# Performance work log

Hardware: AMD Instinct MI355X
Metric: run time of the kernel (lower is better)

Reference implementation:

```python
import jax, jax.numpy as jnp
import numpy as np

B, L, H = 64, 512, 768   # batch, BERT seq len, BERT hidden
D, S, Q = 16, 64, 32     # max_doc_len (sentences), max_seq_len (tokens/sentence), max_query_len
NEG = -900000.0


def setup_inputs() -> dict:
    key = jax.random.key(0)
    k1, k2, k3, k4, k5 = jax.random.split(key, 5)
    rng = np.random.default_rng(0)
    query_len = rng.integers(8, Q + 1, size=B)                 # actual query lengths
    doc_len = rng.integers(4, D + 1, size=B)                   # sentences per doc
    seq_lens = rng.integers(4, 29, size=(B, D))                # tokens per sentence
    seq_lens[np.arange(D)[None, :] >= doc_len[:, None]] = 0    # zero beyond doc_len
    # layout guarantee: 32 + 2 + 16*28 = 482 <= 512
    return {
        "hidden_states": jax.random.normal(k1, (B, L, H), jnp.float32),
        "W_doc": jax.random.normal(k2, (H, 1), jnp.float32) * 0.02,
        "b_doc": jax.random.normal(k3, (1,), jnp.float32) * 0.02,
        "W_query": jax.random.normal(k4, (H, 1), jnp.float32) * 0.02,
        "b_query": jax.random.normal(k5, (1,), jnp.float32) * 0.02,
        "query_len": jnp.asarray(query_len, jnp.int32),
        "seq_lens": jnp.asarray(seq_lens, jnp.int32),
    }


def reference(hidden_states, W_doc, b_doc, W_query, b_query, query_len, seq_lens):
    # --- ragged sentence extraction (vectorized get_sentence_state) ---
    # sentence j of example i starts at query_len[i] + 2 + sum(seq_lens[i,:j])
    offsets = query_len[:, None] + 2 + jnp.cumsum(seq_lens, axis=1) - seq_lens  # [B,D]
    pos = jnp.arange(S, dtype=jnp.int32)
    idx = jnp.clip(offsets[:, :, None] + pos, 0, L - 1)                         # [B,D,S]
    mask_doc = pos[None, None, :] < seq_lens[:, :, None]                        # [B,D,S] bool
    sent = jnp.take_along_axis(hidden_states, idx.reshape(B, D * S, 1), axis=1)
    sent = sent.reshape(B, D, S, H)
    sent = jnp.where(mask_doc[..., None], sent, 0.0)  # zero padding, as original

    # --- masked softmax attention pooling over tokens in each sentence ---
    alpha = (sent @ W_doc + b_doc)[..., 0]                                      # [B,D,S]
    alpha = jnp.where(mask_doc, alpha, NEG)
    alpha = jax.nn.softmax(alpha, axis=-1)
    doc_pooled = jnp.einsum('bds,bdsh->bdh', alpha, sent)                       # [B,D,H]

    # --- ragged query extraction + pooling ---
    q_state = hidden_states[:, 1:1 + Q]                                         # [B,Q,H]
    mask_q = jnp.arange(Q, dtype=jnp.int32)[None, :] < query_len[:, None]       # [B,Q]
    q_state = jnp.where(mask_q[..., None], q_state, 0.0)
    aq = (q_state @ W_query + b_query)[..., 0]                                  # [B,Q]
    aq = jnp.where(mask_q, aq, NEG)
    aq = jax.nn.softmax(aq, axis=-1)
    q_pooled = jnp.einsum('bq,bqh->bh', aq, q_state)                            # [B,H]
    q_bcast = jnp.broadcast_to(q_pooled[:, None, :], doc_pooled.shape)          # [B,D,H]
    return doc_pooled, q_bcast
```

## Files before the change

kernel.cpp:

```cpp
#include <hip/hip_runtime.h>

namespace {
constexpr int Bn = 64;
constexpr int Ln = 512;
constexpr int Hn = 768;
constexpr int Dn = 16;
constexpr int Qn = 32;
constexpr float NEGV = -900000.0f;
}

template<int NIT>
__device__ __forceinline__ void pool_span(
    const float* __restrict__ rowbase,
    const float* __restrict__ W, float bias, int len,
    float* __restrict__ score_sh, float (*pool_sh)[Hn],
    int t, int wave, int lane, float out3[3])
{
    float4 wv[3];
#pragma unroll
    for (int j = 0; j < 3; ++j)
        wv[j] = *reinterpret_cast<const float4*>(W + (lane + 64 * j) * 4);

    float4 c[NIT][3];
#pragma unroll
    for (int it = 0; it < NIT; ++it) {
        const int s = wave + 4 * it;
        if (s < len) {
            const float* r = rowbase + s * Hn;
#pragma unroll
            for (int j = 0; j < 3; ++j)
                c[it][j] = *reinterpret_cast<const float4*>(r + (lane + 64 * j) * 4);
            float p = c[it][0].x * wv[0].x + c[it][0].y * wv[0].y
                    + c[it][0].z * wv[0].z + c[it][0].w * wv[0].w
                    + c[it][1].x * wv[1].x + c[it][1].y * wv[1].y
                    + c[it][1].z * wv[1].z + c[it][1].w * wv[1].w
                    + c[it][2].x * wv[2].x + c[it][2].y * wv[2].y
                    + c[it][2].z * wv[2].z + c[it][2].w * wv[2].w;
#pragma unroll
            for (int off = 32; off; off >>= 1) p += __shfl_down(p, off);
            if (lane == 0) score_sh[s] = p;
        }
    }
    __syncthreads();

    if (t < Qn) {
        const float raw = (t < len) ? (score_sh[t] + bias) : NEGV;
        float m = raw;
#pragma unroll
        for (int off = 16; off; off >>= 1) m = fmaxf(m, __shfl_xor(m, off, 32));
        const float e = expf(raw - m);
        float den = e;
#pragma unroll
        for (int off = 16; off; off >>= 1) den += __shfl_xor(den, off, 32);
        score_sh[t] = (t < len) ? (e / den) : 0.f;
    }
    __syncthreads();

    float4 acc[3];
#pragma unroll
    for (int j = 0; j < 3; ++j) acc[j] = make_float4(0.f, 0.f, 0.f, 0.f);
#pragma unroll
    for (int it = 0; it < NIT; ++it) {
        const int s = wave + 4 * it;
        if (s < len) {
            const float a = score_sh[s];
#pragma unroll
            for (int j = 0; j < 3; ++j) {
                acc[j].x += a * c[it][j].x;
                acc[j].y += a * c[it][j].y;
                acc[j].z += a * c[it][j].z;
                acc[j].w += a * c[it][j].w;
            }
        }
    }

#pragma unroll
    for (int j = 0; j < 3; ++j)
        *reinterpret_cast<float4*>(&pool_sh[wave][(lane + 64 * j) * 4]) = acc[j];
    __syncthreads();
    out3[0] = pool_sh[0][t]       + pool_sh[1][t]       + pool_sh[2][t]       + pool_sh[3][t];
    out3[1] = pool_sh[0][t + 256] + pool_sh[1][t + 256] + pool_sh[2][t + 256] + pool_sh[3][t + 256];
    out3[2] = pool_sh[0][t + 512] + pool_sh[1][t + 512] + pool_sh[2][t + 512] + pool_sh[3][t + 512];
}

__global__ __launch_bounds__(256) void k_fused(
    const float* __restrict__ hs,
    const float* __restrict__ Wd, const float* __restrict__ bd,
    const float* __restrict__ Wq, const float* __restrict__ bq,
    const int* __restrict__ qlen, const int* __restrict__ slens,
    float* __restrict__ out_doc, float* __restrict__ out_q)
{
    __shared__ float score_sh[Qn];
    __shared__ float pool_sh[4][Hn];

    const int t = threadIdx.x;
    const int wave = t >> 6;
    const int lane = t & 63;
    const int bid = blockIdx.x;

    if (bid < Bn) {
        const int b = bid;
        const int ql = qlen[b];
        const float* bp = hs + ((size_t)b * Ln + 1) * Hn;
        float o3[3];
        pool_span<8>(bp, Wq, bq[0], ql, score_sh, pool_sh, t, wave, lane, o3);
        for (int dd = 0; dd < Dn; ++dd) {
            float* o = out_q + ((size_t)b * Dn + dd) * Hn;
            o[t] = o3[0]; o[t + 256] = o3[1]; o[t + 512] = o3[2];
        }
    } else {
        const int id = bid - Bn;
        const int b = id >> 4;
        const int d = id & 15;

        const int sv = slens[b * Dn + (lane & 15)];
        const int sl = __shfl(sv, d, 64);
        float* o = out_doc + ((size_t)b * Dn + d) * Hn;
        if (sl == 0) {
            o[t] = 0.f; o[t + 256] = 0.f; o[t + 512] = 0.f;
            return;
        }
        int pref = 0;
#pragma unroll
        for (int k = 0; k < Dn; ++k)
            pref += (k < d) ? __shfl(sv, k, 64) : 0;
        const int base = qlen[b] + 2 + pref;
        const float* bp = hs + ((size_t)b * Ln + base) * Hn;
        float o3[3];
        pool_span<7>(bp, Wd, bd[0], sl, score_sh, pool_sh, t, wave, lane, o3);
        o[t] = o3[0]; o[t + 256] = o3[1]; o[t + 512] = o3[2];
    }
}

extern "C" void kernel_launch(void* const* d_in, const int* in_sizes, int n_in,
                              void* d_out, int out_size, void* d_ws, size_t ws_size,
                              hipStream_t stream)
{
    const float* hs    = (const float*)d_in[0];
    const float* Wd    = (const float*)d_in[1];
    const float* bd    = (const float*)d_in[2];
    const float* Wq    = (const float*)d_in[3];
    const float* bq    = (const float*)d_in[4];
    const int*   qlen  = (const int*)d_in[5];
    const int*   slens = (const int*)d_in[6];

    float* out_doc = (float*)d_out;
    float* out_q   = out_doc + (size_t)Bn * Dn * Hn;

    k_fused<<<Bn + Bn * Dn, 256, 0, stream>>>(hs, Wd, bd, Wq, bq,
                                              qlen, slens, out_doc, out_q);
}
```

Before: 16.36 us.

## Replace two-pass softmax pooling with per-wave online softmax and merge

Each wave now keeps a running max, running denominator and rescaled accumulator (flash-style online softmax) while streaming its rows. The per-wave partial results are merged through shared memory with exp weights at the end. This removes the score buffer, one block barrier and the register array that held every loaded row, which should lower register pressure and allow more waves in flight. Output stores become float4, but all four waves now write the same full row, so global write traffic is four times larger and that may offset the gain.

```diff
diff --git a/kernel.cpp b/kernel.cpp
--- a/kernel.cpp
+++ b/kernel.cpp
@@ -5,82 +5,76 @@
 constexpr int Ln = 512;
 constexpr int Hn = 768;
 constexpr int Dn = 16;
-constexpr int Qn = 32;
 constexpr float NEGV = -900000.0f;
 }
 
 template<int NIT>
-__device__ __forceinline__ void pool_span(
+__device__ __forceinline__ void flash_span(
     const float* __restrict__ rowbase,
     const float* __restrict__ W, float bias, int len,
-    float* __restrict__ score_sh, float (*pool_sh)[Hn],
-    int t, int wave, int lane, float out3[3])
+    float4 (*pool4)[192], float* m_sh, float* l_sh,
+    int t, int wave, int lane, float4 out4[3])
 {
     float4 wv[3];
 #pragma unroll
     for (int j = 0; j < 3; ++j)
         wv[j] = *reinterpret_cast<const float4*>(W + (lane + 64 * j) * 4);
 
-    float4 c[NIT][3];
+    float4 acc[3];
+#pragma unroll
+    for (int j = 0; j < 3; ++j) acc[j] = make_float4(0.f, 0.f, 0.f, 0.f);
+    float m = -INFINITY, l = 0.f;
+
 #pragma unroll
     for (int it = 0; it < NIT; ++it) {
         const int s = wave + 4 * it;
         if (s < len) {
             const float* r = rowbase + s * Hn;
+            float4 c0 = *reinterpret_cast<const float4*>(r + lane * 4);
+            float4 c1 = *reinterpret_cast<const float4*>(r + (lane + 64) * 4);
+            float4 c2 = *reinterpret_cast<const float4*>(r + (lane + 128) * 4);
+            float p = c0.x * wv[0].x + c0.y * wv[0].y + c0.z * wv[0].z + c0.w * wv[0].w
+                    + c1.x * wv[1].x + c1.y * wv[1].y + c1.z * wv[1].z + c1.w * wv[1].w
+                    + c2.x * wv[2].x + c2.y * wv[2].y + c2.z * wv[2].z + c2.w * wv[2].w;
 #pragma unroll
-            for (int j = 0; j < 3; ++j)
-                c[it][j] = *reinterpret_cast<const float4*>(r + (lane + 64 * j) * 4);
-            float p = c[it][0].x * wv[0].x + c[it][0].y * wv[0].y
-                    + c[it][0].z * wv[0].z + c[it][0].w * wv[0].w
-                    + c[it][1].x * wv[1].x + c[it][1].y * wv[1].y
-                    + c[it][1].z * wv[1].z + c[it][1].w * wv[1].w
-                    + c[it][2].x * wv[2].x + c[it][2].y * wv[2].y
-                    + c[it][2].z * wv[2].z + c[it][2].w * wv[2].w;
-#pragma unroll
-            for (int off = 32; off; off >>= 1) p += __shfl_down(p, off);
-            if (lane == 0) score_sh[s] = p;
-        }
-    }
-    __syncthreads();
-
-    if (t < Qn) {
-        const float raw = (t < len) ? (score_sh[t] + bias) : NEGV;
-        float m = raw;
-#pragma unroll
-        for (int off = 16; off; off >>= 1) m = fmaxf(m, __shfl_xor(m, off, 32));
-        const float e = expf(raw - m);
-        float den = e;
-#pragma unroll
-        for (int off = 16; off; off >>= 1) den += __shfl_xor(den, off, 32);
-        score_sh[t] = (t < len) ? (e / den) : 0.f;
-    }
-    __syncthreads();
-
-    float4 acc[3];
-#pragma unroll
-    for (int j = 0; j < 3; ++j) acc[j] = make_float4(0.f, 0.f, 0.f, 0.f);
-#pragma unroll
-    for (int it = 0; it < NIT; ++it) {
-        const int s = wave + 4 * it;
-        if (s < len) {
-            const float a = score_sh[s];
-#pragma unroll
-            for (int j = 0; j < 3; ++j) {
-                acc[j].x += a * c[it][j].x;
-                acc[j].y += a * c[it][j].y;
-                acc[j].z += a * c[it][j].z;
-                acc[j].w += a * c[it][j].w;
+            for (int off = 32; off; off >>= 1) p += __shfl_xor(p, off);
+            p += bias;
+            if (p > m) {
+                const float sc = __expf(m - p);
+                acc[0].x *= sc; acc[0].y *= sc; acc[0].z *= sc; acc[0].w *= sc;
+                acc[1].x *= sc; acc[1].y *= sc; acc[1].z *= sc; acc[1].w *= sc;
+                acc[2].x *= sc; acc[2].y *= sc; acc[2].z *= sc; acc[2].w *= sc;
+                l *= sc; m = p;
             }
+            const float e = __expf(p - m);
+            acc[0].x += e * c0.x; acc[0].y += e * c0.y; acc[0].z += e * c0.z; acc[0].w += e * c0.w;
+            acc[1].x += e * c1.x; acc[1].y += e * c1.y; acc[1].z += e * c1.z; acc[1].w += e * c1.w;
+            acc[2].x += e * c2.x; acc[2].y += e * c2.y; acc[2].z += e * c2.z; acc[2].w += e * c2.w;
+            l += e;
         }
     }
 
 #pragma unroll
-    for (int j = 0; j < 3; ++j)
-        *reinterpret_cast<float4*>(&pool_sh[wave][(lane + 64 * j) * 4]) = acc[j];
+    for (int j = 0; j < 3; ++j) pool4[wave][lane + 64 * j] = acc[j];
+    if (lane == 0) { m_sh[wave] = m; l_sh[wave] = l; }
     __syncthreads();
-    out3[0] = pool_sh[0][t]       + pool_sh[1][t]       + pool_sh[2][t]       + pool_sh[3][t];
-    out3[1] = pool_sh[0][t + 256] + pool_sh[1][t + 256] + pool_sh[2][t + 256] + pool_sh[3][t + 256];
-    out3[2] = pool_sh[0][t + 512] + pool_sh[1][t + 512] + pool_sh[2][t + 512] + pool_sh[3][t + 512];
+
+    const float m0 = m_sh[0], m1 = m_sh[1], m2 = m_sh[2], m3 = m_sh[3];
+    const float M = fmaxf(fmaxf(m0, m1), fmaxf(m2, m3));
+    const float w0 = __expf(m0 - M), w1 = __expf(m1 - M),
+                w2 = __expf(m2 - M), w3 = __expf(m3 - M);
+    const float L = l_sh[0] * w0 + l_sh[1] * w1 + l_sh[2] * w2 + l_sh[3] * w3;
+    const float inv = 1.f / L;
+#pragma unroll
+    for (int j = 0; j < 3; ++j) {
+        const int col = lane + 64 * j;
+        const float4 s0 = pool4[0][col], s1 = pool4[1][col],
+                     s2 = pool4[2][col], s3 = pool4[3][col];
+        out4[j].x = (s0.x * w0 + s1.x * w1 + s2.x * w2 + s3.x * w3) * inv;
+        out4[j].y = (s0.y * w0 + s1.y * w1 + s2.y * w2 + s3.y * w3) * inv;
+        out4[j].z = (s0.z * w0 + s1.z * w1 + s2.z * w2 + s3.z * w3) * inv;
+        out4[j].w = (s0.w * w0 + s1.w * w1 + s2.w * w2 + s3.w * w3) * inv;
+    }
 }
 
 __global__ __launch_bounds__(256) void k_fused(
@@ -90,8 +84,8 @@
     const int* __restrict__ qlen, const int* __restrict__ slens,
     float* __restrict__ out_doc, float* __restrict__ out_q)
 {
-    __shared__ float score_sh[Qn];
-    __shared__ float pool_sh[4][Hn];
+    __shared__ float4 pool4[4][192];
+    __shared__ float m_sh[4], l_sh[4];
 
     const int t = threadIdx.x;
     const int wave = t >> 6;
@@ -102,11 +96,13 @@
         const int b = bid;
         const int ql = qlen[b];
         const float* bp = hs + ((size_t)b * Ln + 1) * Hn;
-        float o3[3];
-        pool_span<8>(bp, Wq, bq[0], ql, score_sh, pool_sh, t, wave, lane, o3);
+        float4 o4[3];
+        flash_span<8>(bp, Wq, bq[0], ql, pool4, m_sh, l_sh, t, wave, lane, o4);
         for (int dd = 0; dd < Dn; ++dd) {
-            float* o = out_q + ((size_t)b * Dn + dd) * Hn;
-            o[t] = o3[0]; o[t + 256] = o3[1]; o[t + 512] = o3[2];
+            float4* o = reinterpret_cast<float4*>(out_q + ((size_t)b * Dn + dd) * Hn);
+            o[lane]       = o4[0];
+            o[lane + 64]  = o4[1];
+            o[lane + 128] = o4[2];
         }
     } else {
         const int id = bid - Bn;
@@ -115,9 +111,10 @@
 
         const int sv = slens[b * Dn + (lane & 15)];
         const int sl = __shfl(sv, d, 64);
-        float* o = out_doc + ((size_t)b * Dn + d) * Hn;
+        float4* o = reinterpret_cast<float4*>(out_doc + ((size_t)b * Dn + d) * Hn);
         if (sl == 0) {
-            o[t] = 0.f; o[t + 256] = 0.f; o[t + 512] = 0.f;
+            const float4 z = make_float4(0.f, 0.f, 0.f, 0.f);
+            o[lane] = z; o[lane + 64] = z; o[lane + 128] = z;
             return;
         }
         int pref = 0;
@@ -126,9 +123,11 @@
             pref += (k < d) ? __shfl(sv, k, 64) : 0;
         const int base = qlen[b] + 2 + pref;
         const float* bp = hs + ((size_t)b * Ln + base) * Hn;
-        float o3[3];
-        pool_span<7>(bp, Wd, bd[0], sl, score_sh, pool_sh, t, wave, lane, o3);
-        o[t] = o3[0]; o[t + 256] = o3[1]; o[t + 512] = o3[2];
+        float4 o4[3];
+        flash_span<7>(bp, Wd, bd[0], sl, pool4, m_sh, l_sh, t, wave, lane, o4);
+        o[lane]       = o4[0];
+        o[lane + 64]  = o4[1];
+        o[lane + 128] = o4[2];
     }
 }
 
```

New measurement: 25.05 us. 53.1% more time.

## Use 512-thread blocks, register-shuffle softmax weights, and float4 reductions

Applied to the files above, without the earlier changes.

Doubles the block to 8 waves so each wave loads at most 4 rows instead of 7-8, which lowers per-thread register use and gives more memory requests in flight. Every wave now computes the softmax redundantly and broadcasts alpha with a shuffle, removing one barrier and the shared-memory round trip for the weights. The final cross-wave reduction and the output stores use float4 on 192 threads. The risk is fewer resident blocks per CU and an 8-way shared-memory reduction.

```diff
diff --git a/kernel.cpp b/kernel.cpp
--- a/kernel.cpp
+++ b/kernel.cpp
@@ -5,26 +5,67 @@
 constexpr int Ln = 512;
 constexpr int Hn = 768;
 constexpr int Dn = 16;
-constexpr int Qn = 32;
 constexpr float NEGV = -900000.0f;
 }
 
-template<int NIT>
-__device__ __forceinline__ void pool_span(
-    const float* __restrict__ rowbase,
-    const float* __restrict__ W, float bias, int len,
-    float* __restrict__ score_sh, float (*pool_sh)[Hn],
-    int t, int wave, int lane, float out3[3])
+__global__ __launch_bounds__(512) void k_fused(
+    const float* __restrict__ hs,
+    const float* __restrict__ Wd, const float* __restrict__ bd,
+    const float* __restrict__ Wq, const float* __restrict__ bq,
+    const int* __restrict__ qlen, const int* __restrict__ slens,
+    float* __restrict__ out_doc, float* __restrict__ out_q)
 {
+    __shared__ float score_sh[32];
+    __shared__ float4 pool4[8][192];
+
+    const int t = threadIdx.x;
+    const int wave = t >> 6;
+    const int lane = t & 63;
+    const int bid = blockIdx.x;
+
+    const float* rowbase;
+    const float* W;
+    float bias;
+    int len;
+    int b, d = 0;
+    const bool isq = (bid < Bn);
+
+    if (isq) {
+        b = bid;
+        len = qlen[b];
+        W = Wq; bias = bq[0];
+        rowbase = hs + ((size_t)b * Ln + 1) * Hn;
+    } else {
+        const int id = bid - Bn;
+        b = id >> 4;
+        d = id & 15;
+        const int sv = slens[b * Dn + (lane & 15)];
+        len = __shfl(sv, d, 64);
+        if (len == 0) {
+            if (t < 192) {
+                float4* o4 = reinterpret_cast<float4*>(out_doc + ((size_t)b * Dn + d) * Hn);
+                o4[t] = make_float4(0.f, 0.f, 0.f, 0.f);
+            }
+            return;
+        }
+        int pref = 0;
+#pragma unroll
+        for (int k = 0; k < Dn; ++k)
+            pref += (k < d) ? __shfl(sv, k, 64) : 0;
+        const int base = qlen[b] + 2 + pref;
+        W = Wd; bias = bd[0];
+        rowbase = hs + ((size_t)b * Ln + base) * Hn;
+    }
+
     float4 wv[3];
 #pragma unroll
     for (int j = 0; j < 3; ++j)
         wv[j] = *reinterpret_cast<const float4*>(W + (lane + 64 * j) * 4);
 
-    float4 c[NIT][3];
+    float4 c[4][3];
 #pragma unroll
-    for (int it = 0; it < NIT; ++it) {
-        const int s = wave + 4 * it;
+    for (int it = 0; it < 4; ++it) {
+        const int s = wave + 8 * it;
         if (s < len) {
             const float* r = rowbase + s * Hn;
 #pragma unroll
@@ -37,98 +78,60 @@
                     + c[it][2].x * wv[2].x + c[it][2].y * wv[2].y
                     + c[it][2].z * wv[2].z + c[it][2].w * wv[2].w;
 #pragma unroll
-            for (int off = 32; off; off >>= 1) p += __shfl_down(p, off);
+            for (int off = 32; off; off >>= 1) p += __shfl_xor(p, off);
             if (lane == 0) score_sh[s] = p;
         }
     }
     __syncthreads();
 
-    if (t < Qn) {
-        const float raw = (t < len) ? (score_sh[t] + bias) : NEGV;
-        float m = raw;
+    const int si = lane & 31;
+    const float raw = (si < len) ? (score_sh[si] + bias) : NEGV;
+    float mx = raw;
 #pragma unroll
-        for (int off = 16; off; off >>= 1) m = fmaxf(m, __shfl_xor(m, off, 32));
-        const float e = expf(raw - m);
-        float den = e;
+    for (int off = 16; off; off >>= 1) mx = fmaxf(mx, __shfl_xor(mx, off, 32));
+    const float e = __expf(raw - mx);
+    float den = e;
 #pragma unroll
-        for (int off = 16; off; off >>= 1) den += __shfl_xor(den, off, 32);
-        score_sh[t] = (t < len) ? (e / den) : 0.f;
-    }
-    __syncthreads();
+    for (int off = 16; off; off >>= 1) den += __shfl_xor(den, off, 32);
+    const float alpha = (si < len) ? (e / den) : 0.f;
 
     float4 acc[3];
 #pragma unroll
     for (int j = 0; j < 3; ++j) acc[j] = make_float4(0.f, 0.f, 0.f, 0.f);
 #pragma unroll
-    for (int it = 0; it < NIT; ++it) {
-        const int s = wave + 4 * it;
+    for (int it = 0; it < 4; ++it) {
+        const int s = wave + 8 * it;
         if (s < len) {
-            const float a = score_sh[s];
-#pragma unroll
-            for (int j = 0; j < 3; ++j) {
-                acc[j].x += a * c[it][j].x;
-                acc[j].y += a * c[it][j].y;
-                acc[j].z += a * c[it][j].z;
-                acc[j].w += a * c[it][j].w;
-            }
+            const float a = __shfl(alpha, s, 64);
+            acc[0].x += a * c[it][0].x; acc[0].y += a * c[it][0].y;
+            acc[0].z += a * c[it][0].z; acc[0].w += a * c[it][0].w;
+            acc[1].x += a * c[it][1].x; acc[1].y += a * c[it][1].y;
+            acc[1].z += a * c[it][1].z; acc[1].w += a * c[it][1].w;
+            acc[2].x += a * c[it][2].x; acc[2].y += a * c[it][2].y;
+            acc[2].z += a * c[it][2].z; acc[2].w += a * c[it][2].w;
         }
     }
 
 #pragma unroll
-    for (int j = 0; j < 3; ++j)
-        *reinterpret_cast<float4*>(&pool_sh[wave][(lane + 64 * j) * 4]) = acc[j];
+    for (int j = 0; j < 3; ++j) pool4[wave][lane + 64 * j] = acc[j];
     __syncthreads();
-    out3[0] = pool_sh[0][t]       + pool_sh[1][t]       + pool_sh[2][t]       + pool_sh[3][t];
-    out3[1] = pool_sh[0][t + 256] + pool_sh[1][t + 256] + pool_sh[2][t + 256] + pool_sh[3][t + 256];
-    out3[2] = pool_sh[0][t + 512] + pool_sh[1][t + 512] + pool_sh[2][t + 512] + pool_sh[3][t + 512];
-}
 
-__global__ __launch_bounds__(256) void k_fused(
-    const float* __restrict__ hs,
-    const float* __restrict__ Wd, const float* __restrict__ bd,
-    const float* __restrict__ Wq, const float* __restrict__ bq,
-    const int* __restrict__ qlen, const int* __restrict__ slens,
-    float* __restrict__ out_doc, float* __restrict__ out_q)
-{
-    __shared__ float score_sh[Qn];
-    __shared__ float pool_sh[4][Hn];
-
-    const int t = threadIdx.x;
-    const int wave = t >> 6;
-    const int lane = t & 63;
-    const int bid = blockIdx.x;
-
-    if (bid < Bn) {
-        const int b = bid;
-        const int ql = qlen[b];
-        const float* bp = hs + ((size_t)b * Ln + 1) * Hn;
-        float o3[3];
-        pool_span<8>(bp, Wq, bq[0], ql, score_sh, pool_sh, t, wave, lane, o3);
-        for (int dd = 0; dd < Dn; ++dd) {
-            float* o = out_q + ((size_t)b * Dn + dd) * Hn;
-            o[t] = o3[0]; o[t + 256] = o3[1]; o[t + 512] = o3[2];
+    if (t < 192) {
+        float4 r = pool4[0][t];
+#pragma unroll
+        for (int w = 1; w < 8; ++w) {
+            const float4 s = pool4[w][t];
+            r.x += s.x; r.y += s.y; r.z += s.z; r.w += s.w;
         }
-    } else {
-        const int id = bid - Bn;
-        const int b = id >> 4;
-        const int d = id & 15;
-
-        const int sv = slens[b * Dn + (lane & 15)];
-        const int sl = __shfl(sv, d, 64);
-        float* o = out_doc + ((size_t)b * Dn + d) * Hn;
-        if (sl == 0) {
-            o[t] = 0.f; o[t + 256] = 0.f; o[t + 512] = 0.f;
-            return;
+        if (isq) {
+            for (int dd = 0; dd < Dn; ++dd) {
+                float4* o4 = reinterpret_cast<float4*>(out_q + ((size_t)b * Dn + dd) * Hn);
+                o4[t] = r;
+            }
+        } else {
+            float4* o4 = reinterpret_cast<float4*>(out_doc + ((size_t)b * Dn + d) * Hn);
+            o4[t] = r;
         }
-        int pref = 0;
-#pragma unroll
-        for (int k = 0; k < Dn; ++k)
-            pref += (k < d) ? __shfl(sv, k, 64) : 0;
-        const int base = qlen[b] + 2 + pref;
-        const float* bp = hs + ((size_t)b * Ln + base) * Hn;
-        float o3[3];
-        pool_span<7>(bp, Wd, bd[0], sl, score_sh, pool_sh, t, wave, lane, o3);
-        o[t] = o3[0]; o[t + 256] = o3[1]; o[t + 512] = o3[2];
     }
 }
 
@@ -147,6 +150,6 @@
     float* out_doc = (float*)d_out;
     float* out_q   = out_doc + (size_t)Bn * Dn * Hn;
 
-    k_fused<<<Bn + Bn * Dn, 256, 0, stream>>>(hs, Wd, bd, Wq, bq,
+    k_fused<<<Bn + Bn * Dn, 512, 0, stream>>>(hs, Wd, bd, Wq, bq,
                                               qlen, slens, out_doc, out_q);
 }
```

Measured after the change: 17.81 us. 1.09x slower.
